# Kernel optimization log

Hardware: AMD Instinct MI355X
Metric: run time of the kernel (lower is better)

The kernel has to match this reference:

```python
import jax, jax.numpy as jnp
import numpy as np

T_STEPS = 40        # 30 gated steps + 10 extra steps (original while<30 then for min(10,..))
GATED_STEPS = 30
BATCH = 4096
X_DIM = 150
H_DIM = 150


def setup_inputs() -> dict:
    key = jax.random.key(0)
    ks = jax.random.split(key, 11)
    s = lambda k, shape: jax.random.normal(k, shape, jnp.float32) * 0.05
    return {
        "x": jax.random.normal(ks[0], (T_STEPS, BATCH, X_DIM), jnp.float32),
        "w_ih": s(ks[1], (4 * H_DIM, X_DIM)),
        "w_hh": s(ks[2], (4 * H_DIM, H_DIM)),
        "b_ih": s(ks[3], (4 * H_DIM,)),
        "b_hh": s(ks[4], (4 * H_DIM,)),
        "w1": s(ks[5], (50, X_DIM + H_DIM)),
        "b1": s(ks[6], (50,)),
        "w2": s(ks[7], (25, 50)),
        "b2": s(ks[8], (25,)),
        "w3": s(ks[9], (2, 25)),
        "b3": s(ks[10], (2,)),
    }


def reference(x, w_ih, w_hh, b_ih, b_hh, w1, b1, w2, b2, w3, b3):
    B = x.shape[1]
    H = w_hh.shape[1]

    def cell(h, c, xt):
        # PyTorch LSTMCell: gate order i, f, g, o
        g = xt @ w_ih.T + b_ih + h @ w_hh.T + b_hh  # [B, 4H]
        i, f, gg, o = jnp.split(g, 4, axis=-1)
        c = jax.nn.sigmoid(f) * c + jax.nn.sigmoid(i) * jnp.tanh(gg)
        h = jax.nn.sigmoid(o) * jnp.tanh(c)
        return h, c

    def stop_gate(h, xt):
        # original detaches the concat input (requires_grad=False on .data)
        t = jax.lax.stop_gradient(jnp.concatenate([h, xt], axis=-1))  # [B, 300]
        t = jax.nn.relu(t @ w1.T + b1)
        t = jax.nn.relu(t @ w2.T + b2)
        return jax.nn.softmax(jax.nn.relu(t @ w3.T + b3), axis=-1)  # [B, 2]

    def step_gated(carry, xt):
        h, c = carry
        h, c = cell(h, c, xt)
        y = stop_gate(h, xt)
        return (h, c), (h, y)

    def step_plain(carry, xt):
        h, c = carry
        h, c = cell(h, c, xt)
        return (h, c), h

    h0 = jnp.zeros((B, H), x.dtype)
    c0 = jnp.zeros((B, H), x.dtype)
    (h, c), (hs1, ys) = jax.lax.scan(step_gated, (h0, c0), x[:GATED_STEPS])
    outh = h  # h_t at the end of the gated phase (original `outh`)
    (h, c), hs2 = jax.lax.scan(step_plain, (h, c), x[GATED_STEPS:])
    outputs = jnp.concatenate([hs1, hs2], axis=0)  # [T, B, H]
    return outh, outputs, ys
```

## Files before the change

### kernel.cpp

```cpp
#include <hip/hip_runtime.h>
#include <math.h>

#define TSTEPS 40
#define GATED  30
#define BATCH  4096
#define XD     150
#define HD     150
#define HP     160
#define PITCHW 328
#define SXP    328
#define WROWS  704
#define SGP    643
#define ROWS   16
#define NT     512
#define NBLK   (BATCH / ROWS)

#define TCH    4
#define S1P    66
#define S2P    27

#define OFF_OUTPUTS 614400
#define OFF_YS      25190400

typedef float  floatx4 __attribute__((ext_vector_type(4)));
typedef short  shortx8 __attribute__((ext_vector_type(8)));

__device__ __forceinline__ unsigned short bf16_rne(float f) {
    union { float f; unsigned int u; } v; v.f = f;
    unsigned int u = v.u;
    return (unsigned short)((u + 0x7fffu + ((u >> 16) & 1u)) >> 16);
}
__device__ __forceinline__ unsigned int pk2bf(float a, float b) {
    return (unsigned int)bf16_rne(a) | ((unsigned int)bf16_rne(b) << 16);
}
__device__ __forceinline__ float rcp_f(float x) {
    return __builtin_amdgcn_rcpf(x);
}
__device__ __forceinline__ float sigf(float x) {
    return rcp_f(1.0f + __expf(-x));
}
__device__ __forceinline__ float tanh_fast(float x) {
    x = fminf(fmaxf(x, -15.0f), 15.0f);
    float t = __expf(2.0f * x);
    return (t - 1.0f) * rcp_f(t + 1.0f);
}
__device__ __forceinline__ void bar_lds() {
    asm volatile("s_waitcnt lgkmcnt(0)\n\ts_barrier" ::: "memory");
}

__global__ void pack_weights(const float* __restrict__ w_ih, const float* __restrict__ w_hh,
                             const float* __restrict__ b_ih, const float* __restrict__ b_hh,
                             const float* __restrict__ w1,
                             unsigned short* __restrict__ Wc, float* __restrict__ bcp) {
    int idx = blockIdx.x * blockDim.x + threadIdx.x;
    int stride = gridDim.x * blockDim.x;
    for (int i = idx; i < WROWS * PITCHW; i += stride) {
        int j = i / PITCHW, k = i - j * PITCHW;
        float v = 0.0f;
        if (j < 640) {
            int tp = j / HP, u = j - tp * HP;
            if (u < 150) {
                int src = tp * 150 + u;
                if (k < 150)                    v = w_ih[src * 150 + k];
                else if (k >= 160 && k < 310)   v = w_hh[src * 150 + (k - 160)];
            }
        } else {
            int j1 = j - 640;
            if (j1 < 50) {
                if (k < 150)                    v = w1[j1 * 300 + 150 + k];
                else if (k >= 160 && k < 310)   v = w1[j1 * 300 + (k - 160)];
            }
        }
        Wc[i] = bf16_rne(v);
    }
    for (int i = idx; i < 640; i += stride) {
        int tp = i / HP, u = i - tp * HP;
        bcp[i] = (u < 150) ? (b_ih[tp * 150 + u] + b_hh[tp * 150 + u]) : 0.0f;
    }
}

__global__ __launch_bounds__(NT, 2)
void lstm_main(const float* __restrict__ x,
               const unsigned short* __restrict__ Wc,
               const float* __restrict__ bcp, const float* __restrict__ b1,
               const float* __restrict__ w2, const float* __restrict__ b2,
               const float* __restrict__ w3, const float* __restrict__ b3,
               float* __restrict__ outh, float* __restrict__ outputs,
               float* __restrict__ ys) {
    __shared__ unsigned short sxh[ROWS][SXP];
    __shared__ float sg[ROWS][SGP];
    __shared__ unsigned short wlds[8][16][SXP];
    __shared__ float bcs[640], b1s[64];
    __shared__ float sw2[1250], sb2[25], sw3[50], sb3[2];

    unsigned short (*stage4)[SXP] = (unsigned short(*)[SXP])&wlds[0][0][0];
    float (*st1p)[S1P] = (float(*)[S1P])((char*)&wlds[0][0][0] + 41984);
    float (*st2p)[S2P] = (float(*)[S2P])((char*)&wlds[0][0][0] + 58880);

    const int tid  = threadIdx.x;
    const int lane = tid & 63;
    const int wv   = tid >> 6;
    const int lrow = lane & 15;
    const int lq   = lane >> 4;
    const int row0 = blockIdx.x * ROWS;
    const int ET   = 10 * (wv >> 1) + 8 + (wv & 1);

    for (int i = tid; i < ROWS * SXP; i += NT) {
        int r = i / SXP, k = i - r * SXP;
        if (k >= 150) sxh[r][k] = 0;
    }
    for (int i = tid; i < ROWS * 75; i += NT) {
        int rr = i / 75, kk = i - rr * 75;
        float2 v = *(const float2*)(x + ((size_t)row0 + rr) * XD + 2 * kk);
        *(unsigned int*)&sxh[rr][2 * kk] = pk2bf(v.x, v.y);
    }
    for (int i = tid; i < 8 * 16 * 160; i += NT) {
        int w = i / (16 * 160);
        int rem = i - w * (16 * 160);
        int r = rem / 160, k = rem - r * 160;
        int et = 10 * (w >> 1) + 8 + (w & 1);
        *(unsigned int*)&wlds[w][r][2 * k] =
            *(const unsigned int*)&Wc[(size_t)(et * 16 + r) * PITCHW + 2 * k];
    }
    for (int i = tid; i < 640; i += NT) bcs[i] = bcp[i];
    if (tid < 64) b1s[tid] = (tid < 50) ? b1[tid] : 0.0f;
    for (int i = tid; i < 1250; i += NT) sw2[i] = w2[i];
    if (tid < 25) sb2[tid] = b2[tid];
    if (tid < 50) sw3[tid] = w3[tid];
    if (tid < 2)  sb3[tid] = b3[tid];

    shortx8 bfr[40];
#pragma unroll
    for (int j = 0; j < 4; ++j) {
        const unsigned short* wp =
            Wc + (size_t)((10 * j + wv) * 16 + lrow) * PITCHW + lq * 8;
#pragma unroll
        for (int kb = 0; kb < 10; ++kb)
            bfr[j * 10 + kb] = *(const shortx8*)(wp + kb * 32);
    }

    __syncthreads();

    const int uq = wv * 16 + lrow;
    const float bcq0 = bcs[uq];
    const float bcq1 = bcs[160 + uq];
    const float bcq2 = bcs[320 + uq];
    const float bcq3 = bcs[480 + uq];
    const int ue = 128 + (tid & 31);
    const int re = tid >> 5;
    const float bce0 = bcs[ue];
    const float bce1 = bcs[160 + ue];
    const float bce2 = bcs[320 + ue];
    const float bce3 = bcs[480 + ue];
    const int pr0 = tid / 75,          pk0 = tid % 75;
    const int pr1 = (tid + 512) / 75,  pk1 = (tid + 512) % 75;
    const int pr2 = (tid + 1024) / 75, pk2 = (tid + 1024) % 75;

    float cr[4] = {0.f, 0.f, 0.f, 0.f};
    float ce = 0.f;

    for (int t = 0; t < TSTEPS; ++t) {
        float2 px0, px1, px2;
        const bool pf = (t + 1 < TSTEPS);
        if (pf) {
            const float* xn = x + ((size_t)(t + 1) * BATCH + row0) * XD;
            px0 = *(const float2*)(xn + pr0 * XD + 2 * pk0);
            px1 = *(const float2*)(xn + pr1 * XD + 2 * pk1);
            if (tid < 176) px2 = *(const float2*)(xn + pr2 * XD + 2 * pk2);
        }

        floatx4 acc[5];
#pragma unroll
        for (int j = 0; j < 5; ++j) acc[j] = (floatx4){0.f, 0.f, 0.f, 0.f};
#pragma unroll
        for (int kb = 0; kb < 10; ++kb) {
            shortx8 a = *(const shortx8*)&sxh[lrow][kb * 32 + lq * 8];
#pragma unroll
            for (int j = 0; j < 4; ++j)
                acc[j] = __builtin_amdgcn_mfma_f32_16x16x32_bf16(
                    a, bfr[j * 10 + kb], acc[j], 0, 0, 0);
            shortx8 b4 = *(const shortx8*)&wlds[wv][lrow][kb * 32 + lq * 8];
            acc[4] = __builtin_amdgcn_mfma_f32_16x16x32_bf16(a, b4, acc[4], 0, 0, 0);
        }
        {
            const int colb = ET * 16 + lrow;
#pragma unroll
            for (int rg = 0; rg < 4; ++rg)
                sg[lq * 4 + rg][colb] = acc[4][rg];
        }
        bar_lds();

#pragma unroll
        for (int rg = 0; rg < 4; ++rg) {
            float gi = acc[0][rg] + bcq0;
            float gf = acc[1][rg] + bcq1;
            float gg = acc[2][rg] + bcq2;
            float go = acc[3][rg] + bcq3;
            float cn = sigf(gf) * cr[rg] + sigf(gi) * tanh_fast(gg);
            cr[rg] = cn;
            float h = sigf(go) * tanh_fast(cn);
            int r = lq * 4 + rg;
            sxh[r][HP + uq] = bf16_rne(h);
            outputs[((size_t)t * BATCH + row0 + r) * HD + uq] = h;
            if (t == GATED - 1)
                outh[(size_t)(row0 + r) * HD + uq] = h;
        }
        {
            float gi = sg[re][ue]       + bce0;
            float gf = sg[re][160 + ue] + bce1;
            float gg = sg[re][320 + ue] + bce2;
            float go = sg[re][480 + ue] + bce3;
            float cn = sigf(gf) * ce + sigf(gi) * tanh_fast(gg);
            ce = cn;
            float h = sigf(go) * tanh_fast(cn);
            sxh[re][HP + ue] = bf16_rne(h);
            if (ue < 150) {
                outputs[((size_t)t * BATCH + row0 + re) * HD + ue] = h;
                if (t == GATED - 1)
                    outh[(size_t)(row0 + re) * HD + ue] = h;
            }
        }
        if (pf) {
            *(unsigned int*)&sxh[pr0][2 * pk0] = pk2bf(px0.x, px0.y);
            *(unsigned int*)&sxh[pr1][2 * pk1] = pk2bf(px1.x, px1.y);
            if (tid < 176)
                *(unsigned int*)&sxh[pr2][2 * pk2] = pk2bf(px2.x, px2.y);
        }
        bar_lds();
    }

    for (int i = tid; i < TCH * 16 * SXP; i += NT)
        ((unsigned short*)stage4)[i] = 0;
    __syncthreads();

    for (int t0 = 0; t0 < GATED; t0 += TCH) {
        const int tcur = (GATED - t0 < TCH) ? (GATED - t0) : TCH;

        for (int i = tid; i < tcur * 16 * 75; i += NT) {
            int row = i / 75, kk = i - row * 75;
            int r = row & 15, tl = row >> 4;
            size_t base = ((size_t)(t0 + tl) * BATCH + row0 + r) * (size_t)XD;
            float2 xv = *(const float2*)(x + base + 2 * kk);
            float2 hv = *(const float2*)(outputs + base + 2 * kk);
            *(unsigned int*)&stage4[row][2 * kk]      = pk2bf(xv.x, xv.y);
            *(unsigned int*)&stage4[row][HP + 2 * kk] = pk2bf(hv.x, hv.y);
        }
        __syncthreads();

#pragma unroll
        for (int jj = 0; jj < 2; ++jj) {
            int job = wv * 2 + jj;
            int tl = job >> 2, ct = job & 3;
            if (tl < tcur) {
                const unsigned short* wp1 =
                    Wc + (size_t)(640 + ct * 16 + lrow) * PITCHW + lq * 8;
                floatx4 aw = {0.f, 0.f, 0.f, 0.f};
#pragma unroll
                for (int kb = 0; kb < 10; ++kb) {
                    shortx8 a = *(const shortx8*)&stage4[tl * 16 + lrow][kb * 32 + lq * 8];
                    shortx8 b = *(const shortx8*)(wp1 + kb * 32);
                    aw = __builtin_amdgcn_mfma_f32_16x16x32_bf16(a, b, aw, 0, 0, 0);
                }
#pragma unroll
                for (int rg = 0; rg < 4; ++rg)
                    st1p[tl * 16 + lq * 4 + rg][ct * 16 + lrow] = aw[rg];
            }
        }
        __syncthreads();

        for (int e = tid; e < tcur * 16 * 64; e += NT) {
            int s = e >> 6, j = e & 63;
            float v = st1p[s][j] + b1s[j];
            st1p[s][j] = v > 0.0f ? v : 0.0f;
        }
        __syncthreads();

        for (int u = tid; u < tcur * 16 * 25; u += NT) {
            int s = u / 25, j = u - s * 25;
            float a = sb2[j];
            const float* w2r = &sw2[j * 50];
#pragma unroll 10
            for (int k2 = 0; k2 < 50; ++k2)
                a = fmaf(w2r[k2], st1p[s][k2], a);
            st2p[s][j] = a > 0.0f ? a : 0.0f;
        }
        __syncthreads();

        if (tid < tcur * 16) {
            int tl = tid >> 4, r = tid & 15;
            float z0 = sb3[0], z1 = sb3[1];
#pragma unroll
            for (int k2 = 0; k2 < 25; ++k2) {
                z0 = fmaf(sw3[k2],      st2p[tid][k2], z0);
                z1 = fmaf(sw3[25 + k2], st2p[tid][k2], z1);
            }
            z0 = z0 > 0.0f ? z0 : 0.0f;
            z1 = z1 > 0.0f ? z1 : 0.0f;
            float mx = fmaxf(z0, z1);
            float e0 = __expf(z0 - mx), e1 = __expf(z1 - mx);
            float inv = 1.0f / (e0 + e1);
            size_t yb = ((size_t)(t0 + tl) * BATCH + row0 + r) * 2;
            ys[yb]     = e0 * inv;
            ys[yb + 1] = e1 * inv;
        }
        __syncthreads();
    }
}

extern "C" void kernel_launch(void* const* d_in, const int* in_sizes, int n_in,
                              void* d_out, int out_size, void* d_ws, size_t ws_size,
                              hipStream_t stream) {
    const float* x    = (const float*)d_in[0];
    const float* w_ih = (const float*)d_in[1];
    const float* w_hh = (const float*)d_in[2];
    const float* b_ih = (const float*)d_in[3];
    const float* b_hh = (const float*)d_in[4];
    const float* w1   = (const float*)d_in[5];
    const float* b1   = (const float*)d_in[6];
    const float* w2   = (const float*)d_in[7];
    const float* b2   = (const float*)d_in[8];
    const float* w3   = (const float*)d_in[9];
    const float* b3   = (const float*)d_in[10];

    float* out = (float*)d_out;
    unsigned short* Wc  = (unsigned short*)d_ws;
    float*          bcp = (float*)(Wc + WROWS * PITCHW);

    pack_weights<<<256, 256, 0, stream>>>(w_ih, w_hh, b_ih, b_hh, w1, Wc, bcp);

    lstm_main<<<NBLK, NT, 0, stream>>>(
        x, Wc, bcp, b1, w2, b2, w3, b3,
        out, out + OFF_OUTPUTS, out + OFF_YS);
}
```

Before: 321.3 us.

## Double-buffer LSTM hidden-state tile and shrink extra-gate staging buffer

The shared x/h tile becomes two ping-pong buffers, so new h values and the prefetched next x are written into the next buffer while the current one is still read by the MFMAs. This lets the main gate nonlinearity and the x staging run before the first barrier instead of after it. The gate exchange buffer is cut down to only the extra-tile columns, in a padded compact layout, and output pointers are advanced incrementally instead of recomputed each step. Doubling the tile costs extra LDS, which is more than offset by the smaller gate buffer. There are still two barriers per time step.

```diff
diff --git a/kernel.cpp b/kernel.cpp
--- a/kernel.cpp
+++ b/kernel.cpp
@@ -10,7 +10,6 @@
 #define PITCHW 328
 #define SXP    328
 #define WROWS  704
-#define SGP    643
 #define ROWS   16
 #define NT     512
 #define NBLK   (BATCH / ROWS)
@@ -87,8 +86,8 @@
                const float* __restrict__ w3, const float* __restrict__ b3,
                float* __restrict__ outh, float* __restrict__ outputs,
                float* __restrict__ ys) {
-    __shared__ unsigned short sxh[ROWS][SXP];
-    __shared__ float sg[ROWS][SGP];
+    __shared__ unsigned short sxh[2][ROWS][SXP];
+    __shared__ float sge[ROWS][4][33];
     __shared__ unsigned short wlds[8][16][SXP];
     __shared__ float bcs[640], b1s[64];
     __shared__ float sw2[1250], sb2[25], sw3[50], sb3[2];
@@ -103,16 +102,19 @@
     const int lrow = lane & 15;
     const int lq   = lane >> 4;
     const int row0 = blockIdx.x * ROWS;
-    const int ET   = 10 * (wv >> 1) + 8 + (wv & 1);
-
-    for (int i = tid; i < ROWS * SXP; i += NT) {
-        int r = i / SXP, k = i - r * SXP;
-        if (k >= 150) sxh[r][k] = 0;
+    const int ty   = wv >> 1;
+    const int ch   = wv & 1;
+
+    for (int i = tid; i < 2 * ROWS * SXP; i += NT) {
+        int b = i / (ROWS * SXP);
+        int rem = i - b * (ROWS * SXP);
+        int r = rem / SXP, k = rem - r * SXP;
+        if (k >= 150) sxh[b][r][k] = 0;
     }
     for (int i = tid; i < ROWS * 75; i += NT) {
         int rr = i / 75, kk = i - rr * 75;
         float2 v = *(const float2*)(x + ((size_t)row0 + rr) * XD + 2 * kk);
-        *(unsigned int*)&sxh[rr][2 * kk] = pk2bf(v.x, v.y);
+        *(unsigned int*)&sxh[0][rr][2 * kk] = pk2bf(v.x, v.y);
     }
     for (int i = tid; i < 8 * 16 * 160; i += NT) {
         int w = i / (16 * 160);
@@ -146,7 +148,8 @@
     const float bcq1 = bcs[160 + uq];
     const float bcq2 = bcs[320 + uq];
     const float bcq3 = bcs[480 + uq];
-    const int ue = 128 + (tid & 31);
+    const int ce_c = tid & 31;
+    const int ue = 128 + ce_c;
     const int re = tid >> 5;
     const float bce0 = bcs[ue];
     const float bce1 = bcs[160 + ue];
@@ -156,8 +159,14 @@
     const int pr1 = (tid + 512) / 75,  pk1 = (tid + 512) % 75;
     const int pr2 = (tid + 1024) / 75, pk2 = (tid + 1024) % 75;
 
+    float* outc = outputs + (size_t)(row0 + lq * 4) * HD + uq;
+    float* oute = outputs + (size_t)(row0 + re) * HD + ue;
+
     float cr[4] = {0.f, 0.f, 0.f, 0.f};
-    float ce = 0.f;
+    float cex = 0.f;
+
+    unsigned short (*sxc)[SXP] = sxh[0];
+    unsigned short (*sxn)[SXP] = sxh[1];
 
     for (int t = 0; t < TSTEPS; ++t) {
         float2 px0, px1, px2;
@@ -174,7 +183,7 @@
         for (int j = 0; j < 5; ++j) acc[j] = (floatx4){0.f, 0.f, 0.f, 0.f};
 #pragma unroll
         for (int kb = 0; kb < 10; ++kb) {
-            shortx8 a = *(const shortx8*)&sxh[lrow][kb * 32 + lq * 8];
+            shortx8 a = *(const shortx8*)&sxc[lrow][kb * 32 + lq * 8];
 #pragma unroll
             for (int j = 0; j < 4; ++j)
                 acc[j] = __builtin_amdgcn_mfma_f32_16x16x32_bf16(
@@ -182,13 +191,9 @@
             shortx8 b4 = *(const shortx8*)&wlds[wv][lrow][kb * 32 + lq * 8];
             acc[4] = __builtin_amdgcn_mfma_f32_16x16x32_bf16(a, b4, acc[4], 0, 0, 0);
         }
-        {
-            const int colb = ET * 16 + lrow;
-#pragma unroll
-            for (int rg = 0; rg < 4; ++rg)
-                sg[lq * 4 + rg][colb] = acc[4][rg];
-        }
-        bar_lds();
+#pragma unroll
+        for (int rg = 0; rg < 4; ++rg)
+            sge[lq * 4 + rg][ty][ch * 16 + lrow] = acc[4][rg];
 
 #pragma unroll
         for (int rg = 0; rg < 4; ++rg) {
@@ -199,34 +204,39 @@
             float cn = sigf(gf) * cr[rg] + sigf(gi) * tanh_fast(gg);
             cr[rg] = cn;
             float h = sigf(go) * tanh_fast(cn);
-            int r = lq * 4 + rg;
-            sxh[r][HP + uq] = bf16_rne(h);
-            outputs[((size_t)t * BATCH + row0 + r) * HD + uq] = h;
+            sxn[lq * 4 + rg][HP + uq] = bf16_rne(h);
+            outc[rg * HD] = h;
             if (t == GATED - 1)
-                outh[(size_t)(row0 + r) * HD + uq] = h;
-        }
+                outh[(size_t)(row0 + lq * 4 + rg) * HD + uq] = h;
+        }
+        if (pf) {
+            *(unsigned int*)&sxn[pr0][2 * pk0] = pk2bf(px0.x, px0.y);
+            *(unsigned int*)&sxn[pr1][2 * pk1] = pk2bf(px1.x, px1.y);
+            if (tid < 176)
+                *(unsigned int*)&sxn[pr2][2 * pk2] = pk2bf(px2.x, px2.y);
+        }
+        bar_lds();
+
         {
-            float gi = sg[re][ue]       + bce0;
-            float gf = sg[re][160 + ue] + bce1;
-            float gg = sg[re][320 + ue] + bce2;
-            float go = sg[re][480 + ue] + bce3;
-            float cn = sigf(gf) * ce + sigf(gi) * tanh_fast(gg);
-            ce = cn;
+            float gi = sge[re][0][ce_c] + bce0;
+            float gf = sge[re][1][ce_c] + bce1;
+            float gg = sge[re][2][ce_c] + bce2;
+            float go = sge[re][3][ce_c] + bce3;
+            float cn = sigf(gf) * cex + sigf(gi) * tanh_fast(gg);
+            cex = cn;
             float h = sigf(go) * tanh_fast(cn);
-            sxh[re][HP + ue] = bf16_rne(h);
+            sxn[re][HP + ue] = bf16_rne(h);
             if (ue < 150) {
-                outputs[((size_t)t * BATCH + row0 + re) * HD + ue] = h;
+                oute[0] = h;
                 if (t == GATED - 1)
                     outh[(size_t)(row0 + re) * HD + ue] = h;
             }
         }
-        if (pf) {
-            *(unsigned int*)&sxh[pr0][2 * pk0] = pk2bf(px0.x, px0.y);
-            *(unsigned int*)&sxh[pr1][2 * pk1] = pk2bf(px1.x, px1.y);
-            if (tid < 176)
-                *(unsigned int*)&sxh[pr2][2 * pk2] = pk2bf(px2.x, px2.y);
-        }
         bar_lds();
+
+        { unsigned short (*tmp)[SXP] = sxc; sxc = sxn; sxn = tmp; }
+        outc += (size_t)BATCH * HD;
+        oute += (size_t)BATCH * HD;
     }
 
     for (int i = tid; i < TCH * 16 * SXP; i += NT)
```

Result: no change. 318.9 us (-0.7%).
